# Performance work log

Measured on AMD Instinct MI355X. Metric: run time of the kernel, lower is better.

The kernel has to match this reference:

```python
import jax, jax.numpy as jnp
import numpy as np

C = 256
CR = C // 4  # channel_attention_reduce=4


def _dw(x, w, b, ph, pw):
    # depthwise conv, NCHW, kernel w: (C,1,kh,kw)
    y = jax.lax.conv_general_dilated(
        x, w, (1, 1), ((ph, ph), (pw, pw)),
        dimension_numbers=("NCHW", "OIHW", "NCHW"),
        feature_group_count=x.shape[1])
    return y + b[None, :, None, None]


def _conv1x1(x, w, b):
    # w: (Cout, Cin)
    return jnp.einsum("bchw,oc->bohw", x, w) + b[None, :, None, None]


def _channel_att(x, fc1_w, fc1_b, fc2_w, fc2_b):
    def branch(p):  # p: (B, C)
        h = jax.nn.relu(p @ fc1_w.T + fc1_b)
        return jax.nn.sigmoid(h @ fc2_w.T + fc2_b)
    avg = jnp.mean(x, axis=(2, 3))
    mx = jnp.max(x, axis=(2, 3))
    att = branch(avg) + branch(mx)  # (B, C)
    return att[:, :, None, None]


def setup_inputs() -> dict:
    key = jax.random.key(0)
    ks = jax.random.split(key, 24)
    s = 0.05
    d = {
        "x": jax.random.normal(ks[0], (16, C, 56, 56), jnp.float32),
        "conv_w": jax.random.normal(ks[1], (C, C), jnp.float32) * s,
        "conv_b": jax.random.normal(ks[2], (C,), jnp.float32) * s,
        "fc1_w": jax.random.normal(ks[3], (CR, C), jnp.float32) * s,
        "fc1_b": jax.random.normal(ks[4], (CR,), jnp.float32) * s,
        "fc2_w": jax.random.normal(ks[5], (C, CR), jnp.float32) * s,
        "fc2_b": jax.random.normal(ks[6], (C,), jnp.float32) * s,
        "dw5x5_w": jax.random.normal(ks[7], (C, 1, 5, 5), jnp.float32) * s,
        "dw5x5_b": jax.random.normal(ks[8], (C,), jnp.float32) * s,
        "dw1x7_w": jax.random.normal(ks[9], (C, 1, 1, 7), jnp.float32) * s,
        "dw1x7_b": jax.random.normal(ks[10], (C,), jnp.float32) * s,
        "dw7x1_w": jax.random.normal(ks[11], (C, 1, 7, 1), jnp.float32) * s,
        "dw7x1_b": jax.random.normal(ks[12], (C,), jnp.float32) * s,
        "dw1x11_w": jax.random.normal(ks[13], (C, 1, 1, 11), jnp.float32) * s,
        "dw1x11_b": jax.random.normal(ks[14], (C,), jnp.float32) * s,
        "dw11x1_w": jax.random.normal(ks[15], (C, 1, 11, 1), jnp.float32) * s,
        "dw11x1_b": jax.random.normal(ks[16], (C,), jnp.float32) * s,
        "dw1x21_w": jax.random.normal(ks[17], (C, 1, 1, 21), jnp.float32) * s,
        "dw1x21_b": jax.random.normal(ks[18], (C,), jnp.float32) * s,
        "dw21x1_w": jax.random.normal(ks[19], (C, 1, 21, 1), jnp.float32) * s,
        "dw21x1_b": jax.random.normal(ks[20], (C,), jnp.float32) * s,
    }
    return d


def reference(x, conv_w, conv_b, fc1_w, fc1_b, fc2_w, fc2_b,
              dw5x5_w, dw5x5_b, dw1x7_w, dw1x7_b, dw7x1_w, dw7x1_b,
              dw1x11_w, dw1x11_b, dw11x1_w, dw11x1_b,
              dw1x21_w, dw1x21_b, dw21x1_w, dw21x1_b):
    h = jax.nn.gelu(_conv1x1(x, conv_w, conv_b), approximate=False)
    h = _channel_att(h, fc1_w, fc1_b, fc2_w, fc2_b) * h
    x_init = _dw(h, dw5x5_w, dw5x5_b, 2, 2)
    x1 = _dw(_dw(x_init, dw1x7_w, dw1x7_b, 0, 3), dw7x1_w, dw7x1_b, 3, 0)
    x2 = _dw(_dw(x_init, dw1x11_w, dw1x11_b, 0, 5), dw11x1_w, dw11x1_b, 5, 0)
    x3 = _dw(_dw(x_init, dw1x21_w, dw1x21_b, 0, 10), dw21x1_w, dw21x1_b, 10, 0)
    xs = x_init + x1 + x2 + x3
    spatial_att = _conv1x1(xs, conv_w, conv_b)
    out = spatial_att * h
    return _conv1x1(out, conv_w, conv_b)
```

## Files before the change

kernel.cpp:

```cpp
#include <hip/hip_runtime.h>
#include <hip/hip_bf16.h>

#define HW 3136
#define NB 16

typedef float f32x4 __attribute__((ext_vector_type(4)));
typedef float f32x2 __attribute__((ext_vector_type(2)));
typedef short short8 __attribute__((ext_vector_type(8)));
typedef unsigned short ushort8 __attribute__((ext_vector_type(8)));

__device__ inline unsigned short bfb(float f) {
  union { __hip_bfloat16 h; unsigned short u; } cv;
  cv.h = __float2bfloat16(f);
  return cv.u;
}
__device__ inline unsigned pack2(float lo, float hi) {
  return (unsigned)bfb(lo) | ((unsigned)bfb(hi) << 16);
}
__device__ inline unsigned fenc(float f) {
  unsigned u = __float_as_uint(f);
  return (u & 0x80000000u) ? ~u : (u | 0x80000000u);
}
__device__ inline float fdec(unsigned e) {
  return (e & 0x80000000u) ? __uint_as_float(e & 0x7FFFFFFFu) : __uint_as_float(~e);
}
__device__ inline float bf2f(unsigned short u) {
  return __uint_as_float((unsigned)u << 16);
}
__device__ inline float lo16f(unsigned q) { return __uint_as_float(q << 16); }
__device__ inline float hi16f(unsigned q) { return __uint_as_float(q & 0xffff0000u); }

__global__ __launch_bounds__(256) void k0_init(const float* __restrict__ conv_w,
                                               unsigned short* __restrict__ Wbf,
                                               float* __restrict__ psum,
                                               unsigned* __restrict__ pmaxe) {
  int i = blockIdx.x * 256 + threadIdx.x;
  Wbf[i] = bfb(conv_w[i]);
  if (i < 4096) psum[i] = 0.f;
  else if (i < 8192) pmaxe[i - 4096] = 0u;
}

__global__ __launch_bounds__(256) void k1_conv_gelu_pool(
    const float* __restrict__ x, const unsigned short* __restrict__ Wbf,
    const float* __restrict__ conv_b, unsigned short* __restrict__ h_out,
    float* __restrict__ psum, unsigned* __restrict__ pmaxe)
{
  __shared__ __align__(16) unsigned short Xs[256 * 38];
  __shared__ __align__(16) unsigned short Bs[32 * 264];
  const int bid = blockIdx.x;
  const int b = bid / 98, tile = bid - 98 * (bid / 98);
  const int hw0 = tile * 32;
  const int t = threadIdx.x;

  {
    unsigned* Xd = (unsigned*)Xs;
#pragma unroll
    for (int r = 0; r < 8; ++r) {
      int task = t + 256 * r;
      int c = task >> 3, e = task & 7;
      float4 q = *(const float4*)(x + ((size_t)(b * 256 + c)) * HW + hw0 + 4 * e);
      Xd[19 * c + 2 * e]     = pack2(q.x, q.y);
      Xd[19 * c + 2 * e + 1] = pack2(q.z, q.w);
    }
  }
  __syncthreads();

  {
    const unsigned* Xd = (const unsigned*)Xs;
    unsigned* Bd = (unsigned*)Bs;
    int g = t & 127, half = t >> 7;
#pragma unroll
    for (int i = 0; i < 8; ++i) {
      int hp = half * 8 + i;
      unsigned qa = Xd[38 * g + hp];
      unsigned qb = Xd[38 * g + 19 + hp];
      Bd[(2 * hp) * 132 + g]     = (qa & 0xFFFFu) | (qb << 16);
      Bd[(2 * hp + 1) * 132 + g] = (qa >> 16) | (qb & 0xFFFF0000u);
    }
  }
  __syncthreads();

  const int w = t >> 6, l = t & 63, hq = l & 15, g2 = l >> 4;
  const int wm0 = w * 64;
  const f32x4 vzero = {0.f, 0.f, 0.f, 0.f};
  f32x4 acc[4][2];
#pragma unroll
  for (int mi = 0; mi < 4; ++mi)
#pragma unroll
    for (int ni = 0; ni < 2; ++ni) acc[mi][ni] = vzero;

#pragma unroll
  for (int ks = 0; ks < 8; ++ks) {
    short8 a[4], bv[2];
#pragma unroll
    for (int mi = 0; mi < 4; ++mi)
      a[mi] = *(const short8*)(Wbf + (size_t)(wm0 + mi * 16 + hq) * 256 + ks * 32 + g2 * 8);
#pragma unroll
    for (int ni = 0; ni < 2; ++ni)
      bv[ni] = *(const short8*)(Bs + (ni * 16 + hq) * 264 + ks * 32 + g2 * 8);
#pragma unroll
    for (int mi = 0; mi < 4; ++mi)
#pragma unroll
      for (int ni = 0; ni < 2; ++ni)
        acc[mi][ni] = __builtin_amdgcn_mfma_f32_16x16x32_bf16(a[mi], bv[ni], acc[mi][ni], 0, 0, 0);
  }
  __syncthreads();

#pragma unroll
  for (int mi = 0; mi < 4; ++mi) {
#pragma unroll
    for (int r = 0; r < 4; ++r) {
      int o = wm0 + mi * 16 + g2 * 4 + r;
      float bias = conv_b[o];
#pragma unroll
      for (int ni = 0; ni < 2; ++ni) {
        float s = acc[mi][ni][r] + bias;
        float v = 0.5f * s * (1.0f + erff(s * 0.70710678118654752f));
        Bs[(ni * 16 + hq) * 264 + o] = bfb(v);
      }
    }
  }
  __syncthreads();

  {
    const int o = t;
    float sm = 0.f, mx = -1e30f;
    unsigned pk[16];
#pragma unroll
    for (int m = 0; m < 16; ++m) {
      unsigned short r0 = Bs[(2 * m) * 264 + o];
      unsigned short r1 = Bs[(2 * m + 1) * 264 + o];
      float f0 = bf2f(r0), f1 = bf2f(r1);
      sm += f0 + f1;
      mx = fmaxf(mx, fmaxf(f0, f1));
      pk[m] = (unsigned)r0 | ((unsigned)r1 << 16);
    }
    unsigned short* hp = h_out + ((size_t)(b * 256 + o)) * HW + hw0;
#pragma unroll
    for (int q = 0; q < 4; ++q) {
      uint4 s4;
      s4.x = pk[q * 4 + 0]; s4.y = pk[q * 4 + 1]; s4.z = pk[q * 4 + 2]; s4.w = pk[q * 4 + 3];
      *(uint4*)(hp + q * 8) = s4;
    }
    atomicAdd(psum + b * 256 + o, sm);
    atomicMax(pmaxe + b * 256 + o, fenc(mx));
  }
}

__global__ __launch_bounds__(256) void k2_att(
    const float* __restrict__ psum, const unsigned* __restrict__ pmaxe,
    const float* __restrict__ fc1_w, const float* __restrict__ fc1_b,
    const float* __restrict__ fc2_w, const float* __restrict__ fc2_b,
    float* __restrict__ att)
{
  const int b = blockIdx.x, t = threadIdx.x;
  __shared__ float pA[4][64], pM[4][64];
  __shared__ float hA[64], hM[64];
  {
    const int j = t & 63, seg = t >> 6;
    const int base = b * 256 + seg * 64;
    const float* wrow = fc1_w + j * 256 + seg * 64;
    float sA = 0.f, sM = 0.f;
#pragma unroll 8
    for (int c = 0; c < 64; ++c) {
      float wv = wrow[c];
      sA += psum[base + c] * wv;
      sM += fdec(pmaxe[base + c]) * wv;
    }
    pA[seg][j] = sA;
    pM[seg][j] = sM;
  }
  __syncthreads();
  if (t < 64) {
    float a = fc1_b[t] + (pA[0][t] + pA[1][t] + pA[2][t] + pA[3][t]) * (1.f / 3136.f);
    float m = fc1_b[t] + (pM[0][t] + pM[1][t] + pM[2][t] + pM[3][t]);
    hA[t] = fmaxf(a, 0.f);
    hM[t] = fmaxf(m, 0.f);
  }
  __syncthreads();
  float s1 = fc2_b[t], s2 = s1;
#pragma unroll 8
  for (int j = 0; j < 64; ++j) {
    float wv = fc2_w[t * 64 + j];
    s1 += hA[j] * wv;
    s2 += hM[j] * wv;
  }
  att[b * 256 + t] = 1.f / (1.f + expf(-s1)) + 1.f / (1.f + expf(-s2));
}

__global__ __launch_bounds__(256) void k34_dw(
    const unsigned short* __restrict__ h_in, const float* __restrict__ att,
    const float* __restrict__ w5, const float* __restrict__ b5,
    const float* __restrict__ w1x7, const float* __restrict__ b1x7,
    const float* __restrict__ w7x1, const float* __restrict__ b7x1,
    const float* __restrict__ w1x11, const float* __restrict__ b1x11,
    const float* __restrict__ w11x1, const float* __restrict__ b11x1,
    const float* __restrict__ w1x21, const float* __restrict__ b1x21,
    const float* __restrict__ w21x1, const float* __restrict__ b21x1,
    unsigned short* __restrict__ xs_out)
{
  __shared__ __align__(16) unsigned short B0h[4480];
  __shared__ __align__(16) unsigned short T1[62 * 56];
  __shared__ __align__(16) unsigned short T2[66 * 56];
  __shared__ __align__(16) unsigned short T3[76 * 56];
  __shared__ __align__(16) float wk5a[25];
  __shared__ __align__(16) float wk[78];

  const int bid = blockIdx.x;
  const int b = bid >> 8, c = bid & 255;
  const int t = threadIdx.x;
  const size_t plane = (size_t)(b * 256 + c) * HW;
  const float a = att[b * 256 + c];

  if (t < 25) wk5a[t] = w5[c * 25 + t] * a;
  if (t >= 32 && t < 110) {
    int k = t - 32;
    float v;
    if (k < 7) v = w1x7[c * 7 + k];
    else if (k < 14) v = w7x1[c * 7 + k - 7];
    else if (k < 25) v = w1x11[c * 11 + k - 14];
    else if (k < 36) v = w11x1[c * 11 + k - 25];
    else if (k < 57) v = w1x21[c * 21 + k - 36];
    else v = w21x1[c * 21 + k - 57];
    wk[k] = v;
  }
  {
    unsigned* T1d = (unsigned*)T1; unsigned* T2d = (unsigned*)T2; unsigned* T3d = (unsigned*)T3;
    for (int i = t; i < 1008; i += 256) {
      if (i < 84) T1d[i] = 0;
      else if (i < 168) T1d[1652 + i - 84] = 0;
      else if (i < 308) T2d[i - 168] = 0;
      else if (i < 448) T2d[1708 + i - 308] = 0;
      else if (i < 728) T3d[i - 448] = 0;
      else T3d[1848 + i - 728] = 0;
    }
  }
  {
    const unsigned short* hp = h_in + plane;
    unsigned* Bd = (unsigned*)B0h;
    for (int i = t; i < 1800; i += 256) {
      int ly = i / 30, e = i - ly * 30;
      int gy = ly - 2, lx0 = 2 * e - 2;
      unsigned val = 0;
      if ((unsigned)gy < 56u) {
        if (lx0 >= 0 && lx0 + 1 < 56) {
          val = *(const unsigned*)&hp[gy * 56 + lx0];
        } else {
          unsigned short aa = ((unsigned)lx0 < 56u) ? hp[gy * 56 + lx0] : (unsigned short)0;
          unsigned short bb = ((unsigned)(lx0 + 1) < 56u) ? hp[gy * 56 + lx0 + 1] : (unsigned short)0;
          val = (unsigned)aa | ((unsigned)bb << 16);
        }
      }
      Bd[i] = val;
    }
  }
  __syncthreads();

  const int band = t / 14, quad = t - band * 14;
  const int y0 = band * 4, x0 = quad * 4;
  f32x2 aL[4], aH[4];
  {
    const float bias5 = b5[c];
#pragma unroll
    for (int d = 0; d < 4; ++d) {
      aL[d].x = bias5; aL[d].y = bias5;
      aH[d].x = bias5; aH[d].y = bias5;
    }
  }
  if (t < 196) {
    const unsigned* Bd = (const unsigned*)B0h;
#pragma unroll
    for (int r = 0; r < 8; ++r) {
      const int base = (y0 + r) * 30 + 2 * quad;
      uint2 qa = *(const uint2*)(Bd + base);
      uint2 qb = *(const uint2*)(Bd + base + 2);
      uint2 qc = *(const uint2*)(Bd + base + 4);
      float win[10];
      win[0] = lo16f(qa.x); win[1] = hi16f(qa.x);
      win[2] = lo16f(qa.y); win[3] = hi16f(qa.y);
      win[4] = lo16f(qb.x); win[5] = hi16f(qb.x);
      win[6] = lo16f(qb.y); win[7] = hi16f(qb.y);
      win[8] = lo16f(qc.x); win[9] = hi16f(qc.x);
#pragma unroll
      for (int d = 0; d < 4; ++d) {
        const int ky = r - d;
        if (ky < 0 || ky > 4) continue;
#pragma unroll
        for (int kx = 0; kx < 5; ++kx) {
          float wv = wk5a[ky * 5 + kx];
          f32x2 pL; pL.x = win[kx];     pL.y = win[kx + 1];
          f32x2 pH; pH.x = win[kx + 2]; pH.y = win[kx + 3];
          aL[d] = aL[d] + pL * wv;
          aH[d] = aH[d] + pH * wv;
        }
      }
    }
  }
  __syncthreads();

  if (t < 196) {
    unsigned* Bd = (unsigned*)B0h;
#pragma unroll
    for (int d = 0; d < 4; ++d) {
      Bd[(y0 + d) * 40 + 5 + 2 * quad] = pack2(aL[d].x, aL[d].y);
      Bd[(y0 + d) * 40 + 6 + 2 * quad] = pack2(aH[d].x, aH[d].y);
    }
  }
  {
    unsigned* Bd = (unsigned*)B0h;
    for (int i = t; i < 672; i += 256) {
      int y = i / 12, j = i - y * 12;
      int u32col = (j < 5) ? j : (28 + j);
      Bd[y * 40 + u32col] = 0;
    }
  }
  __syncthreads();

  const float bb1 = b1x7[c], bb2 = b1x11[c], bb3 = b1x21[c];
#pragma unroll
  for (int rnd = 0; rnd < 2; ++rnd) {
    if (rnd == 1 && t >= 136) break;
    int tau = t + rnd * 256;
    int y = tau / 7, xa0 = (tau - y * 7) * 8;
    const unsigned* wp = (const unsigned*)B0h + y * 40 + (xa0 >> 1);
    uint4 qa = *(const uint4*)(wp);
    uint4 qb = *(const uint4*)(wp + 4);
    uint4 qc = *(const uint4*)(wp + 8);
    uint2 qd = *(const uint2*)(wp + 12);
    float win[28];
    win[0]  = lo16f(qa.x); win[1]  = hi16f(qa.x);
    win[2]  = lo16f(qa.y); win[3]  = hi16f(qa.y);
    win[4]  = lo16f(qa.z); win[5]  = hi16f(qa.z);
    win[6]  = lo16f(qa.w); win[7]  = hi16f(qa.w);
    win[8]  = lo16f(qb.x); win[9]  = hi16f(qb.x);
    win[10] = lo16f(qb.y); win[11] = hi16f(qb.y);
    win[12] = lo16f(qb.z); win[13] = hi16f(qb.z);
    win[14] = lo16f(qb.w); win[15] = hi16f(qb.w);
    win[16] = lo16f(qc.x); win[17] = hi16f(qc.x);
    win[18] = lo16f(qc.y); win[19] = hi16f(qc.y);
    win[20] = lo16f(qc.z); win[21] = hi16f(qc.z);
    win[22] = lo16f(qc.w); win[23] = hi16f(qc.w);
    win[24] = lo16f(qd.x); win[25] = hi16f(qd.x);
    win[26] = lo16f(qd.y); win[27] = hi16f(qd.y);
    float o1[8], o2[8], o3[8];
#pragma unroll
    for (int d = 0; d < 8; ++d) { o1[d] = bb1; o2[d] = bb2; o3[d] = bb3; }
#pragma unroll
    for (int k = 0; k < 7; ++k) {
      float wv = wk[k];
#pragma unroll
      for (int d = 0; d < 8; ++d) o1[d] += win[d + k + 7] * wv;
    }
#pragma unroll
    for (int k = 0; k < 11; ++k) {
      float wv = wk[14 + k];
#pragma unroll
      for (int d = 0; d < 8; ++d) o2[d] += win[d + k + 5] * wv;
    }
#pragma unroll
    for (int k = 0; k < 21; ++k) {
      float wv = wk[36 + k];
#pragma unroll
      for (int d = 0; d < 8; ++d) o3[d] += win[d + k] * wv;
    }
    uint4 s1, s2, s3;
    s1.x = pack2(o1[0], o1[1]); s1.y = pack2(o1[2], o1[3]); s1.z = pack2(o1[4], o1[5]); s1.w = pack2(o1[6], o1[7]);
    s2.x = pack2(o2[0], o2[1]); s2.y = pack2(o2[2], o2[3]); s2.z = pack2(o2[4], o2[5]); s2.w = pack2(o2[6], o2[7]);
    s3.x = pack2(o3[0], o3[1]); s3.y = pack2(o3[2], o3[3]); s3.z = pack2(o3[4], o3[5]); s3.w = pack2(o3[6], o3[7]);
    *(uint4*)&T1[(y + 3) * 56 + xa0] = s1;
    *(uint4*)&T2[(y + 5) * 56 + xa0] = s2;
    *(uint4*)&T3[(y + 10) * 56 + xa0] = s3;
  }
  __syncthreads();

  const float vb = b7x1[c] + b11x1[c] + b21x1[c];
  unsigned short* op = xs_out + plane;
  if (t < 196) {
    f32x2 rL[4], rH[4];
#pragma unroll
    for (int d = 0; d < 4; ++d) { rL[d] = aL[d] + vb; rH[d] = aH[d] + vb; }
    {
      const unsigned* T1d = (const unsigned*)T1;
#pragma unroll
      for (int j = 0; j < 10; ++j) {
        uint2 q = *(const uint2*)(T1d + (y0 + j) * 28 + 2 * quad);
        f32x2 cL; cL.x = lo16f(q.x); cL.y = hi16f(q.x);
        f32x2 cH; cH.x = lo16f(q.y); cH.y = hi16f(q.y);
#pragma unroll
        for (int d = 0; d < 4; ++d) {
          const int k = j - d;
          if (k < 0 || k > 6) continue;
          float wv = wk[7 + k];
          rL[d] = rL[d] + cL * wv;
          rH[d] = rH[d] + cH * wv;
        }
      }
    }
    {
      const unsigned* T2d = (const unsigned*)T2;
#pragma unroll
      for (int j = 0; j < 14; ++j) {
        uint2 q = *(const uint2*)(T2d + (y0 + j) * 28 + 2 * quad);
        f32x2 cL; cL.x = lo16f(q.x); cL.y = hi16f(q.x);
        f32x2 cH; cH.x = lo16f(q.y); cH.y = hi16f(q.y);
#pragma unroll
        for (int d = 0; d < 4; ++d) {
          const int k = j - d;
          if (k < 0 || k > 10) continue;
          float wv = wk[25 + k];
          rL[d] = rL[d] + cL * wv;
          rH[d] = rH[d] + cH * wv;
        }
      }
    }
    {
      const unsigned* T3d = (const unsigned*)T3;
#pragma unroll
      for (int j = 0; j < 24; ++j) {
        uint2 q = *(const uint2*)(T3d + (y0 + j) * 28 + 2 * quad);
        f32x2 cL; cL.x = lo16f(q.x); cL.y = hi16f(q.x);
        f32x2 cH; cH.x = lo16f(q.y); cH.y = hi16f(q.y);
#pragma unroll
        for (int d = 0; d < 4; ++d) {
          const int k = j - d;
          if (k < 0 || k > 20) continue;
          float wv = wk[57 + k];
          rL[d] = rL[d] + cL * wv;
          rH[d] = rH[d] + cH * wv;
        }
      }
    }
#pragma unroll
    for (int d = 0; d < 4; ++d) {
      uint2 s;
      s.x = pack2(rL[d].x, rL[d].y);
      s.y = pack2(rH[d].x, rH[d].y);
      *(uint2*)&op[(y0 + d) * 56 + x0] = s;
    }
  }
}

__global__ __launch_bounds__(256) void k5_final(
    const unsigned short* __restrict__ xs, const unsigned short* __restrict__ Wbf,
    const float* __restrict__ conv_b, const float* __restrict__ att,
    const unsigned short* __restrict__ h_in, float* __restrict__ outp)
{
  __shared__ __align__(16) unsigned short Bs[64 * 264];
  const int bid = blockIdx.x;
  const int b = bid / 49, tile = bid - 49 * (bid / 49);
  const int hw0 = tile * 64;
  const int t = threadIdx.x;

  {
    int g = t & 127, half = t >> 7;
    const unsigned short* p0 = xs + ((size_t)(b * 256 + 2 * g)) * HW + hw0 + half * 32;
    const unsigned short* p1 = p0 + HW;
    unsigned* Bd = (unsigned*)Bs;
#pragma unroll
    for (int i = 0; i < 32; i += 8) {
      ushort8 a8 = *(const ushort8*)(p0 + i);
      ushort8 c8 = *(const ushort8*)(p1 + i);
      int hw = half * 32 + i;
#pragma unroll
      for (int e = 0; e < 8; ++e)
        Bd[(hw + e) * 132 + g] = (unsigned)a8[e] | ((unsigned)c8[e] << 16);
    }
  }
  __syncthreads();

  const int w = t >> 6, l = t & 63, hq = l & 15, g2 = l >> 4;
  const int wm0 = w * 64;
  const f32x4 vzero = {0.f, 0.f, 0.f, 0.f};
  f32x4 acc[4][4];
#pragma unroll
  for (int mi = 0; mi < 4; ++mi)
#pragma unroll
    for (int ni = 0; ni < 4; ++ni) acc[mi][ni] = vzero;

#pragma unroll
  for (int ks = 0; ks < 8; ++ks) {
    short8 a[4], bv[4];
#pragma unroll
    for (int mi = 0; mi < 4; ++mi)
      a[mi] = *(const short8*)(Wbf + (size_t)(wm0 + mi * 16 + hq) * 256 + ks * 32 + g2 * 8);
#pragma unroll
    for (int ni = 0; ni < 4; ++ni)
      bv[ni] = *(const short8*)(Bs + (ni * 16 + hq) * 264 + ks * 32 + g2 * 8);
#pragma unroll
    for (int mi = 0; mi < 4; ++mi)
#pragma unroll
      for (int ni = 0; ni < 4; ++ni)
        acc[mi][ni] = __builtin_amdgcn_mfma_f32_16x16x32_bf16(a[mi], bv[ni], acc[mi][ni], 0, 0, 0);
  }
  __syncthreads();

#pragma unroll
  for (int mi = 0; mi < 4; ++mi) {
#pragma unroll
    for (int r = 0; r < 4; ++r) {
      int o = wm0 + mi * 16 + g2 * 4 + r;
      float bias = conv_b[o];
      float av = att[b * 256 + o];
      const unsigned short* hp = h_in + ((size_t)(b * 256 + o)) * HW + hw0;
#pragma unroll
      for (int ni = 0; ni < 4; ++ni) {
        float sa = acc[mi][ni][r] + bias;
        float ov = sa * (av * bf2f(hp[ni * 16 + hq]));
        Bs[(ni * 16 + hq) * 264 + o] = bfb(ov);
      }
    }
  }
  __syncthreads();

  f32x4 acc2[4][4];
#pragma unroll
  for (int mi = 0; mi < 4; ++mi)
#pragma unroll
    for (int ni = 0; ni < 4; ++ni) acc2[mi][ni] = vzero;
#pragma unroll
  for (int ks = 0; ks < 8; ++ks) {
    short8 a[4], bv[4];
#pragma unroll
    for (int mi = 0; mi < 4; ++mi)
      a[mi] = *(const short8*)(Wbf + (size_t)(wm0 + mi * 16 + hq) * 256 + ks * 32 + g2 * 8);
#pragma unroll
    for (int ni = 0; ni < 4; ++ni)
      bv[ni] = *(const short8*)(Bs + (ni * 16 + hq) * 264 + ks * 32 + g2 * 8);
#pragma unroll
    for (int mi = 0; mi < 4; ++mi)
#pragma unroll
      for (int ni = 0; ni < 4; ++ni)
        acc2[mi][ni] = __builtin_amdgcn_mfma_f32_16x16x32_bf16(a[mi], bv[ni], acc2[mi][ni], 0, 0, 0);
  }

#pragma unroll
  for (int mi = 0; mi < 4; ++mi) {
#pragma unroll
    for (int r = 0; r < 4; ++r) {
      int o = wm0 + mi * 16 + g2 * 4 + r;
      float bias = conv_b[o];
      float* op = outp + ((size_t)(b * 256 + o)) * HW + hw0;
#pragma unroll
      for (int ni = 0; ni < 4; ++ni) op[ni * 16 + hq] = acc2[mi][ni][r] + bias;
    }
  }
}

extern "C" void kernel_launch(void* const* d_in, const int* in_sizes, int n_in,
                              void* d_out, int out_size, void* d_ws, size_t ws_size,
                              hipStream_t stream) {
  const float* x      = (const float*)d_in[0];
  const float* conv_w = (const float*)d_in[1];
  const float* conv_b = (const float*)d_in[2];
  const float* fc1_w  = (const float*)d_in[3];
  const float* fc1_b  = (const float*)d_in[4];
  const float* fc2_w  = (const float*)d_in[5];
  const float* fc2_b  = (const float*)d_in[6];
  const float* w5     = (const float*)d_in[7];
  const float* b5     = (const float*)d_in[8];
  const float* w1x7   = (const float*)d_in[9];
  const float* b1x7   = (const float*)d_in[10];
  const float* w7x1   = (const float*)d_in[11];
  const float* b7x1   = (const float*)d_in[12];
  const float* w1x11  = (const float*)d_in[13];
  const float* b1x11  = (const float*)d_in[14];
  const float* w11x1  = (const float*)d_in[15];
  const float* b11x1  = (const float*)d_in[16];
  const float* w1x21  = (const float*)d_in[17];
  const float* b1x21  = (const float*)d_in[18];
  const float* w21x1  = (const float*)d_in[19];
  const float* b21x1  = (const float*)d_in[20];
  float* out = (float*)d_out;

  char* ws = (char*)d_ws;
  unsigned short* Wbf = (unsigned short*)(ws);
  float* psum   = (float*)(ws + 131072);
  unsigned* pme = (unsigned*)(ws + 147456);
  float* attb   = (float*)(ws + 163840);
  unsigned short* hbuf = (unsigned short*)(ws + 180224);
  unsigned short* xbuf = (unsigned short*)(ws + 180224 + 25690112);

  k0_init<<<256, 256, 0, stream>>>(conv_w, Wbf, psum, pme);
  k1_conv_gelu_pool<<<1568, 256, 0, stream>>>(x, Wbf, conv_b, hbuf, psum, pme);
  k2_att<<<16, 256, 0, stream>>>(psum, pme, fc1_w, fc1_b, fc2_w, fc2_b, attb);
  k34_dw<<<4096, 256, 0, stream>>>(hbuf, attb, w5, b5, w1x7, b1x7, w7x1, b7x1,
                                   w1x11, b1x11, w11x1, b11x1, w1x21, b1x21,
                                   w21x1, b21x1, xbuf);
  k5_final<<<784, 256, 0, stream>>>(xbuf, Wbf, conv_b, attb, hbuf, out);
}
```

Before: 177.8 us.

## Process depthwise strip branches sequentially through one shared LDS buffer

```diff
diff --git a/kernel.cpp b/kernel.cpp
--- a/kernel.cpp
+++ b/kernel.cpp
@@ -188,135 +188,20 @@
   att[b * 256 + t] = 1.f / (1.f + expf(-s1)) + 1.f / (1.f + expf(-s2));
 }
 
-__global__ __launch_bounds__(256) void k34_dw(
-    const unsigned short* __restrict__ h_in, const float* __restrict__ att,
-    const float* __restrict__ w5, const float* __restrict__ b5,
-    const float* __restrict__ w1x7, const float* __restrict__ b1x7,
-    const float* __restrict__ w7x1, const float* __restrict__ b7x1,
-    const float* __restrict__ w1x11, const float* __restrict__ b1x11,
-    const float* __restrict__ w11x1, const float* __restrict__ b11x1,
-    const float* __restrict__ w1x21, const float* __restrict__ b1x21,
-    const float* __restrict__ w21x1, const float* __restrict__ b21x1,
-    unsigned short* __restrict__ xs_out)
+template<int P, int WOFFH, int WOFFV>
+__device__ __forceinline__ void k34_branch(
+    unsigned short* __restrict__ Tt, const unsigned short* __restrict__ B0h,
+    const float* __restrict__ wk, float bb, int t, int y0, int quad,
+    f32x2* rL, f32x2* rH)
 {
-  __shared__ __align__(16) unsigned short B0h[4480];
-  __shared__ __align__(16) unsigned short T1[62 * 56];
-  __shared__ __align__(16) unsigned short T2[66 * 56];
-  __shared__ __align__(16) unsigned short T3[76 * 56];
-  __shared__ __align__(16) float wk5a[25];
-  __shared__ __align__(16) float wk[78];
-
-  const int bid = blockIdx.x;
-  const int b = bid >> 8, c = bid & 255;
-  const int t = threadIdx.x;
-  const size_t plane = (size_t)(b * 256 + c) * HW;
-  const float a = att[b * 256 + c];
-
-  if (t < 25) wk5a[t] = w5[c * 25 + t] * a;
-  if (t >= 32 && t < 110) {
-    int k = t - 32;
-    float v;
-    if (k < 7) v = w1x7[c * 7 + k];
-    else if (k < 14) v = w7x1[c * 7 + k - 7];
-    else if (k < 25) v = w1x11[c * 11 + k - 14];
-    else if (k < 36) v = w11x1[c * 11 + k - 25];
-    else if (k < 57) v = w1x21[c * 21 + k - 36];
-    else v = w21x1[c * 21 + k - 57];
-    wk[k] = v;
-  }
-  {
-    unsigned* T1d = (unsigned*)T1; unsigned* T2d = (unsigned*)T2; unsigned* T3d = (unsigned*)T3;
-    for (int i = t; i < 1008; i += 256) {
-      if (i < 84) T1d[i] = 0;
-      else if (i < 168) T1d[1652 + i - 84] = 0;
-      else if (i < 308) T2d[i - 168] = 0;
-      else if (i < 448) T2d[1708 + i - 308] = 0;
-      else if (i < 728) T3d[i - 448] = 0;
-      else T3d[1848 + i - 728] = 0;
-    }
-  }
-  {
-    const unsigned short* hp = h_in + plane;
-    unsigned* Bd = (unsigned*)B0h;
-    for (int i = t; i < 1800; i += 256) {
-      int ly = i / 30, e = i - ly * 30;
-      int gy = ly - 2, lx0 = 2 * e - 2;
-      unsigned val = 0;
-      if ((unsigned)gy < 56u) {
-        if (lx0 >= 0 && lx0 + 1 < 56) {
-          val = *(const unsigned*)&hp[gy * 56 + lx0];
-        } else {
-          unsigned short aa = ((unsigned)lx0 < 56u) ? hp[gy * 56 + lx0] : (unsigned short)0;
-          unsigned short bb = ((unsigned)(lx0 + 1) < 56u) ? hp[gy * 56 + lx0 + 1] : (unsigned short)0;
-          val = (unsigned)aa | ((unsigned)bb << 16);
-        }
-      }
-      Bd[i] = val;
-    }
-  }
-  __syncthreads();
-
-  const int band = t / 14, quad = t - band * 14;
-  const int y0 = band * 4, x0 = quad * 4;
-  f32x2 aL[4], aH[4];
-  {
-    const float bias5 = b5[c];
-#pragma unroll
-    for (int d = 0; d < 4; ++d) {
-      aL[d].x = bias5; aL[d].y = bias5;
-      aH[d].x = bias5; aH[d].y = bias5;
-    }
-  }
-  if (t < 196) {
-    const unsigned* Bd = (const unsigned*)B0h;
-#pragma unroll
-    for (int r = 0; r < 8; ++r) {
-      const int base = (y0 + r) * 30 + 2 * quad;
-      uint2 qa = *(const uint2*)(Bd + base);
-      uint2 qb = *(const uint2*)(Bd + base + 2);
-      uint2 qc = *(const uint2*)(Bd + base + 4);
-      float win[10];
-      win[0] = lo16f(qa.x); win[1] = hi16f(qa.x);
-      win[2] = lo16f(qa.y); win[3] = hi16f(qa.y);
-      win[4] = lo16f(qb.x); win[5] = hi16f(qb.x);
-      win[6] = lo16f(qb.y); win[7] = hi16f(qb.y);
-      win[8] = lo16f(qc.x); win[9] = hi16f(qc.x);
-#pragma unroll
-      for (int d = 0; d < 4; ++d) {
-        const int ky = r - d;
-        if (ky < 0 || ky > 4) continue;
-#pragma unroll
-        for (int kx = 0; kx < 5; ++kx) {
-          float wv = wk5a[ky * 5 + kx];
-          f32x2 pL; pL.x = win[kx];     pL.y = win[kx + 1];
-          f32x2 pH; pH.x = win[kx + 2]; pH.y = win[kx + 3];
-          aL[d] = aL[d] + pL * wv;
-          aH[d] = aH[d] + pH * wv;
-        }
-      }
-    }
-  }
-  __syncthreads();
-
-  if (t < 196) {
-    unsigned* Bd = (unsigned*)B0h;
-#pragma unroll
-    for (int d = 0; d < 4; ++d) {
-      Bd[(y0 + d) * 40 + 5 + 2 * quad] = pack2(aL[d].x, aL[d].y);
-      Bd[(y0 + d) * 40 + 6 + 2 * quad] = pack2(aH[d].x, aH[d].y);
-    }
-  }
-  {
-    unsigned* Bd = (unsigned*)B0h;
-    for (int i = t; i < 672; i += 256) {
-      int y = i / 12, j = i - y * 12;
-      int u32col = (j < 5) ? j : (28 + j);
-      Bd[y * 40 + u32col] = 0;
-    }
-  }
-  __syncthreads();
-
-  const float bb1 = b1x7[c], bb2 = b1x11[c], bb3 = b1x21[c];
+  {
+    unsigned* Td = (unsigned*)Tt;
+    for (int i = t; i < 2 * P * 28; i += 256) {
+      int pr = i / 28, e = i - pr * 28;
+      int r = (pr < P) ? pr : (56 + pr);
+      Td[r * 28 + e] = 0;
+    }
+  }
 #pragma unroll
   for (int rnd = 0; rnd < 2; ++rnd) {
     if (rnd == 1 && t >= 136) break;
@@ -342,94 +227,168 @@
     win[22] = lo16f(qc.w); win[23] = hi16f(qc.w);
     win[24] = lo16f(qd.x); win[25] = hi16f(qd.x);
     win[26] = lo16f(qd.y); win[27] = hi16f(qd.y);
-    float o1[8], o2[8], o3[8];
-#pragma unroll
-    for (int d = 0; d < 8; ++d) { o1[d] = bb1; o2[d] = bb2; o3[d] = bb3; }
-#pragma unroll
-    for (int k = 0; k < 7; ++k) {
-      float wv = wk[k];
-#pragma unroll
-      for (int d = 0; d < 8; ++d) o1[d] += win[d + k + 7] * wv;
-    }
-#pragma unroll
-    for (int k = 0; k < 11; ++k) {
-      float wv = wk[14 + k];
-#pragma unroll
-      for (int d = 0; d < 8; ++d) o2[d] += win[d + k + 5] * wv;
-    }
-#pragma unroll
-    for (int k = 0; k < 21; ++k) {
-      float wv = wk[36 + k];
-#pragma unroll
-      for (int d = 0; d < 8; ++d) o3[d] += win[d + k] * wv;
-    }
-    uint4 s1, s2, s3;
-    s1.x = pack2(o1[0], o1[1]); s1.y = pack2(o1[2], o1[3]); s1.z = pack2(o1[4], o1[5]); s1.w = pack2(o1[6], o1[7]);
-    s2.x = pack2(o2[0], o2[1]); s2.y = pack2(o2[2], o2[3]); s2.z = pack2(o2[4], o2[5]); s2.w = pack2(o2[6], o2[7]);
-    s3.x = pack2(o3[0], o3[1]); s3.y = pack2(o3[2], o3[3]); s3.z = pack2(o3[4], o3[5]); s3.w = pack2(o3[6], o3[7]);
-    *(uint4*)&T1[(y + 3) * 56 + xa0] = s1;
-    *(uint4*)&T2[(y + 5) * 56 + xa0] = s2;
-    *(uint4*)&T3[(y + 10) * 56 + xa0] = s3;
-  }
-  __syncthreads();
-
-  const float vb = b7x1[c] + b11x1[c] + b21x1[c];
-  unsigned short* op = xs_out + plane;
+    float o8[8];
+#pragma unroll
+    for (int d = 0; d < 8; ++d) o8[d] = bb;
+#pragma unroll
+    for (int k = 0; k < 2 * P + 1; ++k) {
+      float wv = wk[WOFFH + k];
+#pragma unroll
+      for (int d = 0; d < 8; ++d) o8[d] += win[d + k + (10 - P)] * wv;
+    }
+    uint4 s;
+    s.x = pack2(o8[0], o8[1]); s.y = pack2(o8[2], o8[3]);
+    s.z = pack2(o8[4], o8[5]); s.w = pack2(o8[6], o8[7]);
+    *(uint4*)&Tt[(y + P) * 56 + xa0] = s;
+  }
+  __syncthreads();
   if (t < 196) {
-    f32x2 rL[4], rH[4];
-#pragma unroll
-    for (int d = 0; d < 4; ++d) { rL[d] = aL[d] + vb; rH[d] = aH[d] + vb; }
-    {
-      const unsigned* T1d = (const unsigned*)T1;
-#pragma unroll
-      for (int j = 0; j < 10; ++j) {
-        uint2 q = *(const uint2*)(T1d + (y0 + j) * 28 + 2 * quad);
-        f32x2 cL; cL.x = lo16f(q.x); cL.y = hi16f(q.x);
-        f32x2 cH; cH.x = lo16f(q.y); cH.y = hi16f(q.y);
-#pragma unroll
-        for (int d = 0; d < 4; ++d) {
-          const int k = j - d;
-          if (k < 0 || k > 6) continue;
-          float wv = wk[7 + k];
-          rL[d] = rL[d] + cL * wv;
-          rH[d] = rH[d] + cH * wv;
+    const unsigned* Td = (const unsigned*)Tt;
+#pragma unroll
+    for (int j = 0; j < 4 + 2 * P; ++j) {
+      uint2 q = *(const uint2*)(Td + (y0 + j) * 28 + 2 * quad);
+      f32x2 cL; cL.x = lo16f(q.x); cL.y = hi16f(q.x);
+      f32x2 cH; cH.x = lo16f(q.y); cH.y = hi16f(q.y);
+#pragma unroll
+      for (int d = 0; d < 4; ++d) {
+        const int k = j - d;
+        if (k < 0 || k > 2 * P) continue;
+        float wv = wk[WOFFV + k];
+        rL[d] = rL[d] + cL * wv;
+        rH[d] = rH[d] + cH * wv;
+      }
+    }
+  }
+}
+
+__global__ __launch_bounds__(256) void k34_dw(
+    const unsigned short* __restrict__ h_in, const float* __restrict__ att,
+    const float* __restrict__ w5, const float* __restrict__ b5,
+    const float* __restrict__ w1x7, const float* __restrict__ b1x7,
+    const float* __restrict__ w7x1, const float* __restrict__ b7x1,
+    const float* __restrict__ w1x11, const float* __restrict__ b1x11,
+    const float* __restrict__ w11x1, const float* __restrict__ b11x1,
+    const float* __restrict__ w1x21, const float* __restrict__ b1x21,
+    const float* __restrict__ w21x1, const float* __restrict__ b21x1,
+    unsigned short* __restrict__ xs_out)
+{
+  __shared__ __align__(16) unsigned short B0h[4480];
+  __shared__ __align__(16) unsigned short Tt[76 * 56];
+  __shared__ __align__(16) float wk5a[25];
+  __shared__ __align__(16) float wk[78];
+
+  const int bid = blockIdx.x;
+  const int b = bid >> 8, c = bid & 255;
+  const int t = threadIdx.x;
+  const size_t plane = (size_t)(b * 256 + c) * HW;
+  const float a = att[b * 256 + c];
+
+  if (t < 25) wk5a[t] = w5[c * 25 + t] * a;
+  if (t >= 32 && t < 110) {
+    int k = t - 32;
+    float v;
+    if (k < 7) v = w1x7[c * 7 + k];
+    else if (k < 14) v = w7x1[c * 7 + k - 7];
+    else if (k < 25) v = w1x11[c * 11 + k - 14];
+    else if (k < 36) v = w11x1[c * 11 + k - 25];
+    else if (k < 57) v = w1x21[c * 21 + k - 36];
+    else v = w21x1[c * 21 + k - 57];
+    wk[k] = v;
+  }
+  {
+    const unsigned short* hp = h_in + plane;
+    unsigned* Bd = (unsigned*)B0h;
+    for (int i = t; i < 1800; i += 256) {
+      int ly = i / 30, e = i - ly * 30;
+      int gy = ly - 2, lx0 = 2 * e - 2;
+      unsigned val = 0;
+      if ((unsigned)gy < 56u) {
+        if (lx0 >= 0 && lx0 + 1 < 56) {
+          val = *(const unsigned*)&hp[gy * 56 + lx0];
+        } else {
+          unsigned short aa = ((unsigned)lx0 < 56u) ? hp[gy * 56 + lx0] : (unsigned short)0;
+          unsigned short bb = ((unsigned)(lx0 + 1) < 56u) ? hp[gy * 56 + lx0 + 1] : (unsigned short)0;
+          val = (unsigned)aa | ((unsigned)bb << 16);
         }
       }
-    }
-    {
-      const unsigned* T2d = (const unsigned*)T2;
-#pragma unroll
-      for (int j = 0; j < 14; ++j) {
-        uint2 q = *(const uint2*)(T2d + (y0 + j) * 28 + 2 * quad);
-        f32x2 cL; cL.x = lo16f(q.x); cL.y = hi16f(q.x);
-        f32x2 cH; cH.x = lo16f(q.y); cH.y = hi16f(q.y);
-#pragma unroll
-        for (int d = 0; d < 4; ++d) {
-          const int k = j - d;
-          if (k < 0 || k > 10) continue;
-          float wv = wk[25 + k];
-          rL[d] = rL[d] + cL * wv;
-          rH[d] = rH[d] + cH * wv;
+      Bd[i] = val;
+    }
+  }
+  __syncthreads();
+
+  const int band = t / 14, quad = t - band * 14;
+  const int y0 = band * 4, x0 = quad * 4;
+  f32x2 aL[4], aH[4];
+  {
+    const float bias5 = b5[c];
+#pragma unroll
+    for (int d = 0; d < 4; ++d) {
+      aL[d].x = bias5; aL[d].y = bias5;
+      aH[d].x = bias5; aH[d].y = bias5;
+    }
+  }
+  if (t < 196) {
+    const unsigned* Bd = (const unsigned*)B0h;
+#pragma unroll
+    for (int r = 0; r < 8; ++r) {
+      const int base = (y0 + r) * 30 + 2 * quad;
+      uint2 qa = *(const uint2*)(Bd + base);
+      uint2 qb = *(const uint2*)(Bd + base + 2);
+      uint2 qc = *(const uint2*)(Bd + base + 4);
+      float win[10];
+      win[0] = lo16f(qa.x); win[1] = hi16f(qa.x);
+      win[2] = lo16f(qa.y); win[3] = hi16f(qa.y);
+      win[4] = lo16f(qb.x); win[5] = hi16f(qb.x);
+      win[6] = lo16f(qb.y); win[7] = hi16f(qb.y);
+      win[8] = lo16f(qc.x); win[9] = hi16f(qc.x);
+#pragma unroll
+      for (int d = 0; d < 4; ++d) {
+        const int ky = r - d;
+        if (ky < 0 || ky > 4) continue;
+#pragma unroll
+        for (int kx = 0; kx < 5; ++kx) {
+          float wv = wk5a[ky * 5 + kx];
+          f32x2 pL; pL.x = win[kx];     pL.y = win[kx + 1];
+          f32x2 pH; pH.x = win[kx + 2]; pH.y = win[kx + 3];
+          aL[d] = aL[d] + pL * wv;
+          aH[d] = aH[d] + pH * wv;
         }
       }
     }
-    {
-      const unsigned* T3d = (const unsigned*)T3;
-#pragma unroll
-      for (int j = 0; j < 24; ++j) {
-        uint2 q = *(const uint2*)(T3d + (y0 + j) * 28 + 2 * quad);
-        f32x2 cL; cL.x = lo16f(q.x); cL.y = hi16f(q.x);
-        f32x2 cH; cH.x = lo16f(q.y); cH.y = hi16f(q.y);
-#pragma unroll
-        for (int d = 0; d < 4; ++d) {
-          const int k = j - d;
-          if (k < 0 || k > 20) continue;
-          float wv = wk[57 + k];
-          rL[d] = rL[d] + cL * wv;
-          rH[d] = rH[d] + cH * wv;
-        }
-      }
-    }
+  }
+  __syncthreads();
+
+  if (t < 196) {
+    unsigned* Bd = (unsigned*)B0h;
+#pragma unroll
+    for (int d = 0; d < 4; ++d) {
+      Bd[(y0 + d) * 40 + 5 + 2 * quad] = pack2(aL[d].x, aL[d].y);
+      Bd[(y0 + d) * 40 + 6 + 2 * quad] = pack2(aH[d].x, aH[d].y);
+    }
+  }
+  {
+    unsigned* Bd = (unsigned*)B0h;
+    for (int i = t; i < 672; i += 256) {
+      int y = i / 12, j = i - y * 12;
+      int u32col = (j < 5) ? j : (28 + j);
+      Bd[y * 40 + u32col] = 0;
+    }
+  }
+  __syncthreads();
+
+  const float vb = b7x1[c] + b11x1[c] + b21x1[c];
+  f32x2 rL[4], rH[4];
+#pragma unroll
+  for (int d = 0; d < 4; ++d) { rL[d] = aL[d] + vb; rH[d] = aH[d] + vb; }
+
+  k34_branch<3, 0, 7>(Tt, B0h, wk, b1x7[c], t, y0, quad, rL, rH);
+  __syncthreads();
+  k34_branch<5, 14, 25>(Tt, B0h, wk, b1x11[c], t, y0, quad, rL, rH);
+  __syncthreads();
+  k34_branch<10, 36, 57>(Tt, B0h, wk, b1x21[c], t, y0, quad, rL, rH);
+
+  if (t < 196) {
+    unsigned short* op = xs_out + plane;
 #pragma unroll
     for (int d = 0; d < 4; ++d) {
       uint2 s;
```

Measured after the change: 182.0 us. 1.02x slower.
